# Optimization experiments

Hardware: AMD Instinct MI355X
Metric: run time of the kernel (lower is better)

Reference implementation:

```python
import jax, jax.numpy as jnp
import numpy as np

HEADS = 8
DIM_HEAD = 32
EPS = 1e-5


def setup_inputs() -> dict:
    key = jax.random.key(0)
    ks = jax.random.split(key, 12)
    b, dim, H, W = 16, 256, 64, 64
    led = 128
    hid = HEADS * DIM_HEAD
    return {
        "x": jax.random.normal(ks[0], (b, dim, H, W), dtype=jnp.float32),
        "condition": jax.random.normal(ks[1], (b, led), dtype=jnp.float32),
        "w_qkv": jax.random.normal(ks[2], (3 * hid, dim), dtype=jnp.float32) * 0.02,
        "w_lk": jax.random.normal(ks[3], (hid, led), dtype=jnp.float32) * 0.02,
        "b_lk": jax.random.normal(ks[4], (hid,), dtype=jnp.float32) * 0.02,
        "w_lq": jax.random.normal(ks[5], (hid, led), dtype=jnp.float32) * 0.02,
        "b_lq": jax.random.normal(ks[6], (hid,), dtype=jnp.float32) * 0.02,
        "w_out": jax.random.normal(ks[7], (dim, hid), dtype=jnp.float32) * 0.02,
        "b_out": jax.random.normal(ks[8], (dim,), dtype=jnp.float32) * 0.02,
        "gn_gamma": jnp.ones((dim,), dtype=jnp.float32),
        "gn_beta": jnp.zeros((dim,), dtype=jnp.float32),
    }


def reference(x, condition, w_qkv, w_lk, b_lk, w_lq, b_lq, w_out, b_out, gn_gamma, gn_beta):
    b, c, H, W = x.shape
    n = H * W
    scale = DIM_HEAD ** (-0.5)
    hid = HEADS * DIM_HEAD

    # 1x1 conv QKV projection (no bias)
    qkv = jnp.einsum('oc,bchw->bohw', w_qkv, x)  # [b, 3*hid, H, W]
    qkv = qkv.reshape(b, 3, HEADS, DIM_HEAD, n)
    q, k, v = qkv[:, 0], qkv[:, 1], qkv[:, 2]     # each [b, heads, d, n]

    # conditioning biases
    lk = (condition @ w_lk.T + b_lk).reshape(b, HEADS, DIM_HEAD, 1)
    lq = (condition @ w_lq.T + b_lq).reshape(b, HEADS, DIM_HEAD, 1)
    k = k + lk
    q = q + lq

    # double softmax (linear attention)
    q = jax.nn.softmax(q, axis=-2) * scale  # over feature dim d
    k = jax.nn.softmax(k, axis=-1)          # over spatial dim n

    context = jnp.einsum('bhdn,bhen->bhde', k, v)   # [b, h, d, e]
    out = jnp.einsum('bhde,bhdn->bhen', context, q)  # [b, h, e, n]
    out = out.reshape(b, hid, H, W)

    # to_out: 1x1 conv + bias, then GroupNorm(1, dim)
    y = jnp.einsum('oc,bchw->bohw', w_out, out) + b_out[None, :, None, None]
    mean = jnp.mean(y, axis=(1, 2, 3), keepdims=True)
    var = jnp.var(y, axis=(1, 2, 3), keepdims=True)
    y = (y - mean) * jax.lax.rsqrt(var + EPS)
    return y * gn_gamma[None, :, None, None] + gn_beta[None, :, None, None]
```

## Files before the change

kernel.cpp:

```cpp
#include <hip/hip_runtime.h>


#define NB    16
#define DIM   256
#define NSP   4096
#define LED   128
#define HID   256
#define NHEAD 8
#define SCALE 0.17677669529663687f

typedef __bf16 bf16x8 __attribute__((ext_vector_type(8)));
typedef float f32x4 __attribute__((ext_vector_type(4)));
typedef unsigned short us8 __attribute__((ext_vector_type(8)));
typedef unsigned short us4 __attribute__((ext_vector_type(4)));

__device__ __forceinline__ unsigned short f2bf(float f){
  unsigned u = __builtin_bit_cast(unsigned, f);
  u += 0x7fffu + ((u >> 16) & 1u);
  return (unsigned short)(u >> 16);
}
__device__ __forceinline__ float bf2f(unsigned short h){
  unsigned u = ((unsigned)h) << 16;
  return __builtin_bit_cast(float, u);
}
__device__ __forceinline__ bf16x8 ldb8(const unsigned short* p){
  us8 r = *(const us8*)p;
  return __builtin_bit_cast(bf16x8, r);
}
__device__ __forceinline__ f32x4 mfma16(bf16x8 a, bf16x8 b, f32x4 c){
  return __builtin_amdgcn_mfma_f32_16x16x32_bf16(a, b, c, 0, 0, 0);
}
__device__ __forceinline__ void gl16(const unsigned short* g, unsigned short* l){
  __builtin_amdgcn_global_load_lds(
      (const __attribute__((address_space(1))) unsigned int*)g,
      (__attribute__((address_space(3))) unsigned int*)l,
      16, 0, 0);
}

__global__ __launch_bounds__(256) void k0_prep(
    const float* __restrict__ wqkv, const float* __restrict__ cond,
    const float* __restrict__ wlk, const float* __restrict__ blk,
    const float* __restrict__ wlq, const float* __restrict__ blq,
    unsigned short* __restrict__ whi,
    float* __restrict__ lk, float* __restrict__ lq)
{
  const int idx = blockIdx.x*256 + threadIdx.x;
  if (idx < 768*256){
    whi[idx] = f2bf(wqkv[idx]);
  } else {
    int i = idx - 768*256;
    const int which = (i >= NB*HID) ? 1 : 0;
    i &= (NB*HID - 1);
    const int b = i >> 8, o = i & 255;
    const float* wm = which ? wlq : wlk;
    const float* bs = which ? blq : blk;
    float s = bs[o];
    const float* c = cond + b*LED;
    const float* wr = wm + o*LED;
    for (int j=0;j<LED;j++) s += c[j]*wr[j];
    (which ? lq : lk)[i] = s;
  }
}

__global__ __launch_bounds__(256) void k1_txpose(
    const float* __restrict__ x, unsigned short* __restrict__ xt)
{
  __shared__ float tile[64][65];
  const int c0 = blockIdx.x*64, n0 = blockIdx.y*64, b = blockIdx.z;
  const int t = threadIdx.x;
  const int tr = t >> 6, tc = t & 63;
  const float* xp = x + ((size_t)b*DIM + c0)*NSP + n0;
  #pragma unroll
  for (int i=0;i<16;i++){
    const int cl = i*4 + tr;
    tile[cl][tc] = xp[(size_t)cl*NSP + tc];
  }
  __syncthreads();
  unsigned short* xtp = xt + ((size_t)b*NSP + n0)*DIM + c0;
  #pragma unroll
  for (int pass=0; pass<2; pass++){
    const int nl = pass*32 + (t>>3);
    const int c8 = (t&7)*8;
    us8 v;
    #pragma unroll
    for (int j=0;j<8;j++) v[j] = f2bf(tile[c8+j][nl]);
    *(us8*)&xtp[(size_t)nl*DIM + c8] = v;
  }
}

__global__ __launch_bounds__(256) void k2_gemm1(
    const unsigned short* __restrict__ whi,
    const unsigned short* __restrict__ xt,
    const float* __restrict__ lkv, const float* __restrict__ lqv,
    unsigned short* __restrict__ qh,
    unsigned short* __restrict__ kexp, unsigned short* __restrict__ vout,
    float* __restrict__ ksum)
{
  __shared__ __align__(16) unsigned char smraw[32768];
  unsigned short* Ah  = (unsigned short*)smraw;
  unsigned short* Bt  = (unsigned short*)(smraw + 16384);
  unsigned short* stg = (unsigned short*)smraw;

  const int nt = blockIdx.x, mt = blockIdx.y, b = blockIdx.z;
  const int o0 = mt*128, n0 = nt*128;
  const int t = threadIdx.x, lane = t & 63, wv = t >> 6;
  const int wr = wv >> 1, wc = wv & 1;
  const int cl = lane & 15, g = lane >> 4;

  f32x4 acc[4][4];
  const f32x4 z4 = {0.f,0.f,0.f,0.f};
  #pragma unroll
  for (int m=0;m<4;m++)
    #pragma unroll
    for (int n=0;n<4;n++) acc[m][n] = z4;

  const unsigned short* xb = xt + ((size_t)b*NSP + n0)*DIM;
  const int rowc = lane >> 3;
  const int gcol = 8*((lane & 7) ^ rowc);

  for (int kt=0; kt<4; kt++){
    const int k0 = kt*64;
    __syncthreads();
    #pragma unroll
    for (int j=0;j<4;j++){
      const int rg = wv*4 + j;
      const int rr = rg*8 + rowc;
      gl16(&whi[(size_t)(o0+rr)*DIM + k0 + gcol], &Ah[rg*512]);
      gl16(&xb [(size_t)rr*DIM      + k0 + gcol], &Bt[rg*512]);
    }
    __syncthreads();
    #pragma unroll
    for (int kk=0; kk<2; kk++){
      const int ko = kk*32 + g*8;
      const int kosw = ko ^ ((cl & 7) << 3);
      bf16x8 a1[4], bb[4];
      #pragma unroll
      for (int m=0;m<4;m++)
        a1[m] = ldb8(&Ah[(wr*64 + m*16 + cl)*64 + kosw]);
      #pragma unroll
      for (int n=0;n<4;n++)
        bb[n] = ldb8(&Bt[(wc*64 + n*16 + cl)*64 + kosw]);
      #pragma unroll
      for (int m=0;m<4;m++)
        #pragma unroll
        for (int n=0;n<4;n++)
          acc[m][n] = mfma16(a1[m], bb[n], acc[m][n]);
    }
  }

  __syncthreads();

  if (mt < 2){
    float lqr[4][4];
    #pragma unroll
    for (int m=0;m<4;m++)
      #pragma unroll
      for (int i=0;i<4;i++)
        lqr[m][i] = lqv[b*HID + o0 + wr*64 + m*16 + g*4 + i];
    #pragma unroll
    for (int j=0;j<2;j++){
      #pragma unroll
      for (int nf=0;nf<4;nf++){
        float e[8]; float mx = -1e30f;
        #pragma unroll
        for (int mm=0;mm<2;mm++)
          #pragma unroll
          for (int i=0;i<4;i++){
            const int m = 2*j+mm;
            const float v = acc[m][nf][i] + lqr[m][i];
            e[mm*4+i] = v; mx = fmaxf(mx, v);
          }
        mx = fmaxf(mx, __shfl_xor(mx, 16));
        mx = fmaxf(mx, __shfl_xor(mx, 32));
        float s = 0.f;
        #pragma unroll
        for (int q2=0;q2<8;q2++){ e[q2] = __expf(e[q2]-mx); s += e[q2]; }
        s += __shfl_xor(s, 16);
        s += __shfl_xor(s, 32);
        const float r = 1.f/s;
        const int n_local = wc*64 + nf*16 + cl;
        const int rsw = (n_local & 7) << 3;
        #pragma unroll
        for (int mm=0;mm<2;mm++){
          const int dg_local = wr*64 + (2*j+mm)*16 + g*4;
          us4 h4;
          #pragma unroll
          for (int i=0;i<4;i++) h4[i] = f2bf(e[mm*4+i]*r);
          *(us4*)&stg[n_local*128 + (dg_local ^ rsw)] = h4;
        }
      }
    }
    __syncthreads();
    unsigned short* qbase = qh + ((size_t)b*NSP + n0)*HID + o0;
    #pragma unroll
    for (int i2=0;i2<8;i2++){
      const int n_local = wv*32 + i2*4 + (lane>>4);
      const int dg8 = (lane&15)*8;
      us8 val = *(const us8*)&stg[n_local*128 + (dg8 ^ ((n_local&7)<<3))];
      *(us8*)&qbase[(size_t)n_local*HID + dg8] = val;
    }
  } else {
    const int isK = (mt < 4);
    const int dgbase = isK ? (mt-2)*128 : (mt-4)*128;
    #pragma unroll
    for (int m=0;m<4;m++)
      #pragma unroll
      for (int i=0;i<4;i++){
        const int dg_local = wr*64 + m*16 + g*4 + i;
        const int nb0 = wc*64 + cl;
        const int rsw = (dg_local & 7) << 3;
        if (isK){
          const float lkval = lkv[b*HID + dgbase + dg_local];
          float s = 0.f;
          #pragma unroll
          for (int nf=0;nf<4;nf++){
            const float v = __expf(acc[m][nf][i] + lkval);
            const unsigned short hh = f2bf(v);
            stg[dg_local*128 + ((nb0 + nf*16) ^ rsw)] = hh;
            s += bf2f(hh);
          }
          s += __shfl_xor(s,1); s += __shfl_xor(s,2);
          s += __shfl_xor(s,4); s += __shfl_xor(s,8);
          if (cl == 0) atomicAdd(&ksum[b*HID + dgbase + dg_local], s);
        } else {
          #pragma unroll
          for (int nf=0;nf<4;nf++)
            stg[dg_local*128 + ((nb0 + nf*16) ^ rsw)] = f2bf(acc[m][nf][i]);
        }
      }
    __syncthreads();
    unsigned short* obase = (isK ? kexp : vout) + ((size_t)b*HID + dgbase)*NSP + n0;
    #pragma unroll
    for (int i2=0;i2<8;i2++){
      const int dg_local = wv*32 + i2*4 + (lane>>4);
      const int n8 = (lane&15)*8;
      us8 val = *(const us8*)&stg[dg_local*128 + (n8 ^ ((dg_local&7)<<3))];
      *(us8*)&obase[(size_t)dg_local*NSP + n8] = val;
    }
  }
}

__global__ __launch_bounds__(256) void k3_ctx(
    const unsigned short* __restrict__ kexp, const unsigned short* __restrict__ vv,
    float* __restrict__ ctxp)
{
  const int half = blockIdx.x, h = blockIdx.y, b = blockIdx.z;
  const int t = threadIdx.x, lane = t&63, wv = t>>6;
  const int cl = lane&15, g = lane>>4;
  const int nstart = half*2048 + wv*512;
  f32x4 acc[2][2];
  const f32x4 z4 = {0.f,0.f,0.f,0.f};
  acc[0][0]=z4; acc[0][1]=z4; acc[1][0]=z4; acc[1][1]=z4;
  const unsigned short* kb = kexp + ((size_t)b*HID + h*32)*NSP;
  const unsigned short* vb = vv   + ((size_t)b*HID + h*32)*NSP;
  for (int ks=0; ks<16; ks++){
    const int k = nstart + ks*32 + g*8;
    bf16x8 a0 = ldb8(&kb[(size_t)(cl)   *NSP + k]);
    bf16x8 a1 = ldb8(&kb[(size_t)(16+cl)*NSP + k]);
    bf16x8 b0 = ldb8(&vb[(size_t)(cl)   *NSP + k]);
    bf16x8 b1 = ldb8(&vb[(size_t)(16+cl)*NSP + k]);
    acc[0][0] = mfma16(a0,b0,acc[0][0]);
    acc[0][1] = mfma16(a0,b1,acc[0][1]);
    acc[1][0] = mfma16(a1,b0,acc[1][0]);
    acc[1][1] = mfma16(a1,b1,acc[1][1]);
  }
  float* outp = ctxp + ((((size_t)b*NHEAD + h)*2 + half)*4 + wv)*1024;
  #pragma unroll
  for (int dm=0;dm<2;dm++)
    #pragma unroll
    for (int em=0;em<2;em++)
      #pragma unroll
      for (int i=0;i<4;i++)
        outp[(dm*16 + g*4 + i)*32 + em*16 + cl] = acc[dm][em][i];
}

__global__ __launch_bounds__(256) void k4_m(
    const float* __restrict__ ctxp, const float* __restrict__ ksum,
    const float* __restrict__ wout,
    unsigned short* __restrict__ mhi)
{
  const int h = blockIdx.x, b = blockIdx.y;
  __shared__ float ctxl[32][32];
  __shared__ float rkn[32];
  const int t = threadIdx.x;
  const float* base = ctxp + (((size_t)b*NHEAD + h)*8)*1024;
  #pragma unroll
  for (int r=0;r<4;r++){
    const int de = r*256 + t;
    float s = 0.f;
    #pragma unroll
    for (int p=0;p<8;p++) s += base[p*1024 + de];
    ctxl[de>>5][de&31] = s;
  }
  if (t < 32) rkn[t] = SCALE / ksum[b*HID + h*32 + t];
  __syncthreads();
  float w[32];
  const float* wrow = wout + (size_t)t*HID + h*32;
  #pragma unroll
  for (int el=0;el<32;el++) w[el] = wrow[el];
  for (int dl=0; dl<32; dl++){
    float s = 0.f;
    #pragma unroll
    for (int el=0;el<32;el++) s += w[el]*ctxl[dl][el];
    s *= rkn[dl];
    mhi[((size_t)b*HID + t)*HID + h*32 + dl] = f2bf(s);
  }
}

__global__ __launch_bounds__(256) void k5a_stats(
    const unsigned short* __restrict__ mhi,
    const unsigned short* __restrict__ qhp, const float* __restrict__ bout,
    float* __restrict__ bsum, float* __restrict__ bssq)
{
  __shared__ __align__(16) unsigned char smraw[32768];
  unsigned short* Ah = (unsigned short*)smraw;
  unsigned short* Bh = (unsigned short*)(smraw + 16384);
  __shared__ float red[8];

  const int nt = blockIdx.x, mt = blockIdx.y, b = blockIdx.z;
  const int o0 = mt*128, n0 = nt*128;
  const int t = threadIdx.x, lane = t&63, wv = t>>6;
  const int wr = wv>>1, wc = wv&1;
  const int cl = lane&15, g = lane>>4;

  f32x4 acc[4][4];
  const f32x4 z4 = {0.f,0.f,0.f,0.f};
  #pragma unroll
  for (int m=0;m<4;m++)
    #pragma unroll
    for (int n=0;n<4;n++) acc[m][n] = z4;

  const unsigned short* ab_h = mhi + (size_t)b*HID*HID;
  const unsigned short* bb_h = qhp + ((size_t)b*NSP + n0)*HID;
  const int rowc = lane >> 3;
  const int gcol = 8*((lane & 7) ^ rowc);

  for (int kt=0; kt<4; kt++){
    const int k0 = kt*64;
    __syncthreads();
    #pragma unroll
    for (int j=0;j<4;j++){
      const int rg = wv*4 + j;
      const int rr = rg*8 + rowc;
      gl16(&ab_h[(size_t)(o0+rr)*HID + k0 + gcol], &Ah[rg*512]);
      gl16(&bb_h[(size_t)rr*HID      + k0 + gcol], &Bh[rg*512]);
    }
    __syncthreads();
    #pragma unroll
    for (int kk=0;kk<2;kk++){
      const int ko = kk*32 + g*8;
      const int kosw = ko ^ ((cl & 7) << 3);
      bf16x8 ah[4], bh[4];
      #pragma unroll
      for (int m=0;m<4;m++)
        ah[m] = ldb8(&Ah[(wr*64 + m*16 + cl)*64 + kosw]);
      #pragma unroll
      for (int n=0;n<4;n++)
        bh[n] = ldb8(&Bh[(wc*64 + n*16 + cl)*64 + kosw]);
      #pragma unroll
      for (int m=0;m<4;m++)
        #pragma unroll
        for (int n=0;n<4;n++)
          acc[m][n] = mfma16(ah[m], bh[n], acc[m][n]);
    }
  }

  float lsum = 0.f, lss = 0.f;
  #pragma unroll
  for (int m=0;m<4;m++)
    #pragma unroll
    for (int i=0;i<4;i++){
      const float bo = bout[o0 + wr*64 + m*16 + g*4 + i];
      #pragma unroll
      for (int nf=0;nf<4;nf++){
        const float v = acc[m][nf][i] + bo;
        lsum += v; lss += v*v;
      }
    }
  #pragma unroll
  for (int sft=1; sft<64; sft<<=1){
    lsum += __shfl_xor(lsum, sft);
    lss  += __shfl_xor(lss,  sft);
  }
  if (lane == 0){ red[wv] = lsum; red[4+wv] = lss; }
  __syncthreads();
  if (t == 0){
    atomicAdd(&bsum[b], red[0]+red[1]+red[2]+red[3]);
    atomicAdd(&bssq[b], red[4]+red[5]+red[6]+red[7]);
  }
}

__global__ __launch_bounds__(256) void k5b_write(
    const unsigned short* __restrict__ mhi,
    const unsigned short* __restrict__ qhp, const float* __restrict__ bout,
    const float* __restrict__ bsum, const float* __restrict__ bssq,
    const float* __restrict__ gamma, const float* __restrict__ beta,
    float* __restrict__ out)
{
  __shared__ __align__(16) unsigned char smraw[32768];
  unsigned short* Ah = (unsigned short*)smraw;
  unsigned short* Bh = (unsigned short*)(smraw + 16384);
  float* stg = (float*)smraw;

  const int nt = blockIdx.x, mt = blockIdx.y, b = blockIdx.z;
  const int o0 = mt*128, n0 = nt*128;
  const int t = threadIdx.x, lane = t&63, wv = t>>6;
  const int wr = wv>>1, wc = wv&1;
  const int cl = lane&15, g = lane>>4;

  f32x4 acc[4][4];
  const f32x4 z4 = {0.f,0.f,0.f,0.f};
  #pragma unroll
  for (int m=0;m<4;m++)
    #pragma unroll
    for (int n=0;n<4;n++) acc[m][n] = z4;

  const unsigned short* ab_h = mhi + (size_t)b*HID*HID;
  const unsigned short* bb_h = qhp + ((size_t)b*NSP + n0)*HID;
  const int rowc = lane >> 3;
  const int gcol = 8*((lane & 7) ^ rowc);

  for (int kt=0; kt<4; kt++){
    const int k0 = kt*64;
    __syncthreads();
    #pragma unroll
    for (int j=0;j<4;j++){
      const int rg = wv*4 + j;
      const int rr = rg*8 + rowc;
      gl16(&ab_h[(size_t)(o0+rr)*HID + k0 + gcol], &Ah[rg*512]);
      gl16(&bb_h[(size_t)rr*HID      + k0 + gcol], &Bh[rg*512]);
    }
    __syncthreads();
    #pragma unroll
    for (int kk=0;kk<2;kk++){
      const int ko = kk*32 + g*8;
      const int kosw = ko ^ ((cl & 7) << 3);
      bf16x8 ah[4], bh[4];
      #pragma unroll
      for (int m=0;m<4;m++)
        ah[m] = ldb8(&Ah[(wr*64 + m*16 + cl)*64 + kosw]);
      #pragma unroll
      for (int n=0;n<4;n++)
        bh[n] = ldb8(&Bh[(wc*64 + n*16 + cl)*64 + kosw]);
      #pragma unroll
      for (int m=0;m<4;m++)
        #pragma unroll
        for (int n=0;n<4;n++)
          acc[m][n] = mfma16(ah[m], bh[n], acc[m][n]);
    }
  }

  const float inv = 1.f/1048576.f;
  const float mean = bsum[b]*inv;
  const float var  = bssq[b]*inv - mean*mean;
  const float ri = rsqrtf(var + 1e-5f);
  float gav[4][4], bev[4][4];
  #pragma unroll
  for (int m=0;m<4;m++)
    #pragma unroll
    for (int i=0;i<4;i++){
      const int o = o0 + wr*64 + m*16 + g*4 + i;
      const float ga = gamma[o]*ri;
      gav[m][i] = ga;
      bev[m][i] = beta[o] + (bout[o]-mean)*ga;
    }

  #pragma unroll
  for (int p=0;p<2;p++){
    __syncthreads();
    #pragma unroll
    for (int mm=0;mm<2;mm++){
      const int m = 2*p+mm;
      #pragma unroll
      for (int nf=0;nf<4;nf++)
        #pragma unroll
        for (int i=0;i<4;i++){
          const int lr = wr*32 + mm*16 + g*4 + i;
          const int col = wc*64 + nf*16 + cl;
          stg[lr*128 + (col ^ ((lr&7)<<2))] = acc[m][nf][i]*gav[m][i] + bev[m][i];
        }
    }
    __syncthreads();
    #pragma unroll
    for (int i2=0;i2<8;i2++){
      const int lr = wv*16 + i2*2 + (lane>>5);
      const int colw = (lane&31)*4;
      f32x4 v = *(const f32x4*)&stg[lr*128 + (colw ^ ((lr&7)<<2))];
      const int dg = o0 + (lr>>5)*64 + p*32 + (lr&31);
      *(f32x4*)&out[((size_t)b*HID + dg)*NSP + n0 + colw] = v;
    }
  }
}

#define OFF_XT     0ull
#define OFF_QH     33554432ull
#define OFF_CTXP   67108864ull
#define OFF_MH     71303168ull
#define OFF_LK     73400320ull
#define OFF_LQ     73416704ull
#define OFF_WHI    73433088ull
#define OFF_KSUM   73826304ull
#define OFF_BSUM   73842688ull
#define OFF_BSSQ   73842752ull

extern "C" void kernel_launch(void* const* d_in, const int* in_sizes, int n_in,
                              void* d_out, int out_size, void* d_ws, size_t ws_size,
                              hipStream_t stream) {
  const float* x     = (const float*)d_in[0];
  const float* cond  = (const float*)d_in[1];
  const float* wqkv  = (const float*)d_in[2];
  const float* wlk   = (const float*)d_in[3];
  const float* blk   = (const float*)d_in[4];
  const float* wlq   = (const float*)d_in[5];
  const float* blq   = (const float*)d_in[6];
  const float* wout  = (const float*)d_in[7];
  const float* bout  = (const float*)d_in[8];
  const float* gamma = (const float*)d_in[9];
  const float* beta  = (const float*)d_in[10];

  char* ws = (char*)d_ws;
  unsigned short* xt   = (unsigned short*)(ws + OFF_XT);
  unsigned short* qh   = (unsigned short*)(ws + OFF_QH);
  float*          ctxp = (float*)(ws + OFF_CTXP);
  unsigned short* mhi  = (unsigned short*)(ws + OFF_MH);
  float*          lk   = (float*)(ws + OFF_LK);
  float*          lq   = (float*)(ws + OFF_LQ);
  unsigned short* whi  = (unsigned short*)(ws + OFF_WHI);
  float*          ksum = (float*)(ws + OFF_KSUM);
  float*          bsum = (float*)(ws + OFF_BSUM);
  float*          bssq = (float*)(ws + OFF_BSSQ);

  unsigned short* kexp = (unsigned short*)d_out;
  unsigned short* vscr = (unsigned short*)d_out + 16777216;
  float*          y    = (float*)d_out;

  hipMemsetAsync(ws + OFF_KSUM, 0, 16384 + 128, stream);

  k0_prep  <<<800, 256, 0, stream>>>(wqkv, cond, wlk, blk, wlq, blq, whi, lk, lq);
  k1_txpose<<<dim3(4,64,16), 256, 0, stream>>>(x, xt);
  k2_gemm1 <<<dim3(32,6,16), 256, 0, stream>>>(whi, xt, lk, lq, qh, kexp, vscr, ksum);
  k3_ctx   <<<dim3(2,8,16), 256, 0, stream>>>(kexp, vscr, ctxp);
  k4_m     <<<dim3(8,16), 256, 0, stream>>>(ctxp, ksum, wout, mhi);
  k5a_stats<<<dim3(32,2,16), 256, 0, stream>>>(mhi, qh, bout, bsum, bssq);
  k5b_write<<<dim3(32,2,16), 256, 0, stream>>>(mhi, qh, bout, bsum, bssq, gamma, beta, y);
}
```

Baseline: 154.4 us.

## Double-buffer LDS tiles with K=32 steps in three GEMM kernels

Replaces the single-buffered K=64 staging loop in the QKV GEMM, stats GEMM and write GEMM with a two-buffer K=32 pipeline. The next tile's global-to-LDS load is issued before the MFMAs on the current buffer, and a new XOR swizzle fits the narrower 32-column rows. This aims to overlap global load latency with compute and cut one barrier per step. In exchange it doubles the loop trip count and relies on the async load completing before the barrier.

```diff
diff --git a/kernel.cpp b/kernel.cpp
--- a/kernel.cpp
+++ b/kernel.cpp
@@ -97,8 +97,6 @@
     float* __restrict__ ksum)
 {
   __shared__ __align__(16) unsigned char smraw[32768];
-  unsigned short* Ah  = (unsigned short*)smraw;
-  unsigned short* Bt  = (unsigned short*)(smraw + 16384);
   unsigned short* stg = (unsigned short*)smraw;
 
   const int nt = blockIdx.x, mt = blockIdx.y, b = blockIdx.z;
@@ -115,40 +113,43 @@
     for (int n=0;n<4;n++) acc[m][n] = z4;
 
   const unsigned short* xb = xt + ((size_t)b*NSP + n0)*DIM;
-  const int rowc = lane >> 3;
-  const int gcol = 8*((lane & 7) ^ rowc);
-
-  for (int kt=0; kt<4; kt++){
-    const int k0 = kt*64;
-    __syncthreads();
-    #pragma unroll
-    for (int j=0;j<4;j++){
-      const int rg = wv*4 + j;
-      const int rr = rg*8 + rowc;
-      gl16(&whi[(size_t)(o0+rr)*DIM + k0 + gcol], &Ah[rg*512]);
-      gl16(&xb [(size_t)rr*DIM      + k0 + gcol], &Bt[rg*512]);
-    }
-    __syncthreads();
-    #pragma unroll
-    for (int kk=0; kk<2; kk++){
-      const int ko = kk*32 + g*8;
-      const int kosw = ko ^ ((cl & 7) << 3);
-      bf16x8 a1[4], bb[4];
-      #pragma unroll
-      for (int m=0;m<4;m++)
-        a1[m] = ldb8(&Ah[(wr*64 + m*16 + cl)*64 + kosw]);
+  const int gc = (((lane&3) ^ ((lane>>2)&3) ^ ((lane>>4)&3)) << 3);
+  const int lrow = lane >> 2;
+  const int psw = ((g ^ (cl&3) ^ (cl>>2)) << 3);
+
+  auto stage = [&](int kt, int sel){
+    unsigned short* Ab = (unsigned short*)(smraw + sel*16384);
+    unsigned short* Bb = Ab + 4096;
+    const int k0 = kt*32;
+    #pragma unroll
+    for (int j=0;j<2;j++){
+      const int rg = wv*2 + j;
+      const int rr = rg*16 + lrow;
+      gl16(&whi[(size_t)(o0+rr)*DIM + k0 + gc], &Ab[rg*512]);
+      gl16(&xb [(size_t)rr*DIM      + k0 + gc], &Bb[rg*512]);
+    }
+  };
+
+  stage(0, 0);
+  __syncthreads();
+  for (int kt=0; kt<8; kt++){
+    if (kt < 7) stage(kt+1, (kt+1)&1);
+    const unsigned short* Ab = (const unsigned short*)(smraw + (kt&1)*16384);
+    const unsigned short* Bb = Ab + 4096;
+    bf16x8 a1[4], bb[4];
+    #pragma unroll
+    for (int m=0;m<4;m++)
+      a1[m] = ldb8(&Ab[(wr*64 + m*16 + cl)*32 + psw]);
+    #pragma unroll
+    for (int n=0;n<4;n++)
+      bb[n] = ldb8(&Bb[(wc*64 + n*16 + cl)*32 + psw]);
+    #pragma unroll
+    for (int m=0;m<4;m++)
       #pragma unroll
       for (int n=0;n<4;n++)
-        bb[n] = ldb8(&Bt[(wc*64 + n*16 + cl)*64 + kosw]);
-      #pragma unroll
-      for (int m=0;m<4;m++)
-        #pragma unroll
-        for (int n=0;n<4;n++)
-          acc[m][n] = mfma16(a1[m], bb[n], acc[m][n]);
-    }
-  }
-
-  __syncthreads();
+        acc[m][n] = mfma16(a1[m], bb[n], acc[m][n]);
+    __syncthreads();
+  }
 
   if (mt < 2){
     float lqr[4][4];
@@ -313,8 +314,6 @@
     float* __restrict__ bsum, float* __restrict__ bssq)
 {
   __shared__ __align__(16) unsigned char smraw[32768];
-  unsigned short* Ah = (unsigned short*)smraw;
-  unsigned short* Bh = (unsigned short*)(smraw + 16384);
   __shared__ float red[8];
 
   const int nt = blockIdx.x, mt = blockIdx.y, b = blockIdx.z;
@@ -332,37 +331,42 @@
 
   const unsigned short* ab_h = mhi + (size_t)b*HID*HID;
   const unsigned short* bb_h = qhp + ((size_t)b*NSP + n0)*HID;
-  const int rowc = lane >> 3;
-  const int gcol = 8*((lane & 7) ^ rowc);
-
-  for (int kt=0; kt<4; kt++){
-    const int k0 = kt*64;
-    __syncthreads();
-    #pragma unroll
-    for (int j=0;j<4;j++){
-      const int rg = wv*4 + j;
-      const int rr = rg*8 + rowc;
-      gl16(&ab_h[(size_t)(o0+rr)*HID + k0 + gcol], &Ah[rg*512]);
-      gl16(&bb_h[(size_t)rr*HID      + k0 + gcol], &Bh[rg*512]);
-    }
-    __syncthreads();
-    #pragma unroll
-    for (int kk=0;kk<2;kk++){
-      const int ko = kk*32 + g*8;
-      const int kosw = ko ^ ((cl & 7) << 3);
-      bf16x8 ah[4], bh[4];
-      #pragma unroll
-      for (int m=0;m<4;m++)
-        ah[m] = ldb8(&Ah[(wr*64 + m*16 + cl)*64 + kosw]);
+  const int gc = (((lane&3) ^ ((lane>>2)&3) ^ ((lane>>4)&3)) << 3);
+  const int lrow = lane >> 2;
+  const int psw = ((g ^ (cl&3) ^ (cl>>2)) << 3);
+
+  auto stage = [&](int kt, int sel){
+    unsigned short* Ab = (unsigned short*)(smraw + sel*16384);
+    unsigned short* Bb = Ab + 4096;
+    const int k0 = kt*32;
+    #pragma unroll
+    for (int j=0;j<2;j++){
+      const int rg = wv*2 + j;
+      const int rr = rg*16 + lrow;
+      gl16(&ab_h[(size_t)(o0+rr)*HID + k0 + gc], &Ab[rg*512]);
+      gl16(&bb_h[(size_t)rr*HID      + k0 + gc], &Bb[rg*512]);
+    }
+  };
+
+  stage(0, 0);
+  __syncthreads();
+  for (int kt=0; kt<8; kt++){
+    if (kt < 7) stage(kt+1, (kt+1)&1);
+    const unsigned short* Ab = (const unsigned short*)(smraw + (kt&1)*16384);
+    const unsigned short* Bb = Ab + 4096;
+    bf16x8 ah[4], bh[4];
+    #pragma unroll
+    for (int m=0;m<4;m++)
+      ah[m] = ldb8(&Ab[(wr*64 + m*16 + cl)*32 + psw]);
+    #pragma unroll
+    for (int n=0;n<4;n++)
+      bh[n] = ldb8(&Bb[(wc*64 + n*16 + cl)*32 + psw]);
+    #pragma unroll
+    for (int m=0;m<4;m++)
       #pragma unroll
       for (int n=0;n<4;n++)
-        bh[n] = ldb8(&Bh[(wc*64 + n*16 + cl)*64 + kosw]);
-      #pragma unroll
-      for (int m=0;m<4;m++)
-        #pragma unroll
-        for (int n=0;n<4;n++)
-          acc[m][n] = mfma16(ah[m], bh[n], acc[m][n]);
-    }
+        acc[m][n] = mfma16(ah[m], bh[n], acc[m][n]);
+    __syncthreads();
   }
 
   float lsum = 0.f, lss = 0.f;
@@ -398,8 +402,6 @@
     float* __restrict__ out)
 {
   __shared__ __align__(16) unsigned char smraw[32768];
-  unsigned short* Ah = (unsigned short*)smraw;
-  unsigned short* Bh = (unsigned short*)(smraw + 16384);
   float* stg = (float*)smraw;
 
   const int nt = blockIdx.x, mt = blockIdx.y, b = blockIdx.z;
@@ -417,37 +419,42 @@
 
   const unsigned short* ab_h = mhi + (size_t)b*HID*HID;
   const unsigned short* bb_h = qhp + ((size_t)b*NSP + n0)*HID;
-  const int rowc = lane >> 3;
-  const int gcol = 8*((lane & 7) ^ rowc);
-
-  for (int kt=0; kt<4; kt++){
-    const int k0 = kt*64;
-    __syncthreads();
-    #pragma unroll
-    for (int j=0;j<4;j++){
-      const int rg = wv*4 + j;
-      const int rr = rg*8 + rowc;
-      gl16(&ab_h[(size_t)(o0+rr)*HID + k0 + gcol], &Ah[rg*512]);
-      gl16(&bb_h[(size_t)rr*HID      + k0 + gcol], &Bh[rg*512]);
-    }
-    __syncthreads();
-    #pragma unroll
-    for (int kk=0;kk<2;kk++){
-      const int ko = kk*32 + g*8;
-      const int kosw = ko ^ ((cl & 7) << 3);
-      bf16x8 ah[4], bh[4];
-      #pragma unroll
-      for (int m=0;m<4;m++)
-        ah[m] = ldb8(&Ah[(wr*64 + m*16 + cl)*64 + kosw]);
+  const int gc = (((lane&3) ^ ((lane>>2)&3) ^ ((lane>>4)&3)) << 3);
+  const int lrow = lane >> 2;
+  const int psw = ((g ^ (cl&3) ^ (cl>>2)) << 3);
+
+  auto stage = [&](int kt, int sel){
+    unsigned short* Ab = (unsigned short*)(smraw + sel*16384);
+    unsigned short* Bb = Ab + 4096;
+    const int k0 = kt*32;
+    #pragma unroll
+    for (int j=0;j<2;j++){
+      const int rg = wv*2 + j;
+      const int rr = rg*16 + lrow;
+      gl16(&ab_h[(size_t)(o0+rr)*HID + k0 + gc], &Ab[rg*512]);
+      gl16(&bb_h[(size_t)rr*HID      + k0 + gc], &Bb[rg*512]);
+    }
+  };
+
+  stage(0, 0);
+  __syncthreads();
+  for (int kt=0; kt<8; kt++){
+    if (kt < 7) stage(kt+1, (kt+1)&1);
+    const unsigned short* Ab = (const unsigned short*)(smraw + (kt&1)*16384);
+    const unsigned short* Bb = Ab + 4096;
+    bf16x8 ah[4], bh[4];
+    #pragma unroll
+    for (int m=0;m<4;m++)
+      ah[m] = ldb8(&Ab[(wr*64 + m*16 + cl)*32 + psw]);
+    #pragma unroll
+    for (int n=0;n<4;n++)
+      bh[n] = ldb8(&Bb[(wc*64 + n*16 + cl)*32 + psw]);
+    #pragma unroll
+    for (int m=0;m<4;m++)
       #pragma unroll
       for (int n=0;n<4;n++)
-        bh[n] = ldb8(&Bh[(wc*64 + n*16 + cl)*64 + kosw]);
-      #pragma unroll
-      for (int m=0;m<4;m++)
-        #pragma unroll
-        for (int n=0;n<4;n++)
-          acc[m][n] = mfma16(ah[m], bh[n], acc[m][n]);
-    }
+        acc[m][n] = mfma16(ah[m], bh[n], acc[m][n]);
+    __syncthreads();
   }
 
   const float inv = 1.f/1048576.f;
```

Result: no change. 157.5 us (+2.0%).

## Fuse K/V projection with context computation, keeping K and V in LDS

Applied to the files above, without the earlier changes.

The fused QKV GEMM is split into a Q-only kernel and a K/V kernel. For each 128-column spatial tile, the K/V kernel computes exp(K) and V, stages both in LDS and immediately forms per-tile partial context matrices with MFMA. This drops the global write and read of the bf16 K and V tensors and removes the separate context kernel. In exchange the context partials grow to 32 per head, which k4 now reduces, and the K/V kernel uses 64 KB of LDS, which lowers occupancy.

```diff
diff --git a/kernel.cpp b/kernel.cpp
--- a/kernel.cpp
+++ b/kernel.cpp
@@ -88,13 +88,11 @@
   }
 }
 
-__global__ __launch_bounds__(256) void k2_gemm1(
+__global__ __launch_bounds__(256) void k2q_gemm1(
     const unsigned short* __restrict__ whi,
     const unsigned short* __restrict__ xt,
-    const float* __restrict__ lkv, const float* __restrict__ lqv,
-    unsigned short* __restrict__ qh,
-    unsigned short* __restrict__ kexp, unsigned short* __restrict__ vout,
-    float* __restrict__ ksum)
+    const float* __restrict__ lqv,
+    unsigned short* __restrict__ qh)
 {
   __shared__ __align__(16) unsigned char smraw[32768];
   unsigned short* Ah  = (unsigned short*)smraw;
@@ -150,128 +148,182 @@
 
   __syncthreads();
 
-  if (mt < 2){
-    float lqr[4][4];
+  float lqr[4][4];
+  #pragma unroll
+  for (int m=0;m<4;m++)
+    #pragma unroll
+    for (int i=0;i<4;i++)
+      lqr[m][i] = lqv[b*HID + o0 + wr*64 + m*16 + g*4 + i];
+  #pragma unroll
+  for (int j=0;j<2;j++){
+    #pragma unroll
+    for (int nf=0;nf<4;nf++){
+      float e[8]; float mx = -1e30f;
+      #pragma unroll
+      for (int mm=0;mm<2;mm++)
+        #pragma unroll
+        for (int i=0;i<4;i++){
+          const int m = 2*j+mm;
+          const float v = acc[m][nf][i] + lqr[m][i];
+          e[mm*4+i] = v; mx = fmaxf(mx, v);
+        }
+      mx = fmaxf(mx, __shfl_xor(mx, 16));
+      mx = fmaxf(mx, __shfl_xor(mx, 32));
+      float s = 0.f;
+      #pragma unroll
+      for (int q2=0;q2<8;q2++){ e[q2] = __expf(e[q2]-mx); s += e[q2]; }
+      s += __shfl_xor(s, 16);
+      s += __shfl_xor(s, 32);
+      const float r = 1.f/s;
+      const int n_local = wc*64 + nf*16 + cl;
+      const int rsw = (n_local & 7) << 3;
+      #pragma unroll
+      for (int mm=0;mm<2;mm++){
+        const int dg_local = wr*64 + (2*j+mm)*16 + g*4;
+        us4 h4;
+        #pragma unroll
+        for (int i=0;i<4;i++) h4[i] = f2bf(e[mm*4+i]*r);
+        *(us4*)&stg[n_local*128 + (dg_local ^ rsw)] = h4;
+      }
+    }
+  }
+  __syncthreads();
+  unsigned short* qbase = qh + ((size_t)b*NSP + n0)*HID + o0;
+  #pragma unroll
+  for (int i2=0;i2<8;i2++){
+    const int n_local = wv*32 + i2*4 + (lane>>4);
+    const int dg8 = (lane&15)*8;
+    us8 val = *(const us8*)&stg[n_local*128 + (dg8 ^ ((n_local&7)<<3))];
+    *(us8*)&qbase[(size_t)n_local*HID + dg8] = val;
+  }
+}
+
+__global__ __launch_bounds__(256) void k2_kv(
+    const unsigned short* __restrict__ whi,
+    const unsigned short* __restrict__ xt,
+    const float* __restrict__ lkv,
+    float* __restrict__ ksum, float* __restrict__ ctxp)
+{
+  __shared__ __align__(16) unsigned char smraw[65536];
+  unsigned short* Abuf = (unsigned short*)smraw;
+  unsigned short* Bbuf = (unsigned short*)(smraw + 16384);
+  unsigned short* Kstg = (unsigned short*)(smraw + 32768);
+  unsigned short* Vstg = (unsigned short*)smraw;
+
+  const int nt = blockIdx.x, hq = blockIdx.y, b = blockIdx.z;
+  const int n0 = nt*128;
+  const int t = threadIdx.x, lane = t & 63, wv = t >> 6;
+  const int wr = wv >> 1, wc = wv & 1;
+  const int cl = lane & 15, g = lane >> 4;
+
+  const unsigned short* xb = xt + ((size_t)b*NSP + n0)*DIM;
+  const int rowc = lane >> 3;
+  const int gcol = 8*((lane & 7) ^ rowc);
+
+  for (int panel=0; panel<2; ++panel){
+    const int prow = 256 + panel*256 + hq*128;
+    f32x4 acc[4][4];
+    const f32x4 z4 = {0.f,0.f,0.f,0.f};
     #pragma unroll
     for (int m=0;m<4;m++)
       #pragma unroll
-      for (int i=0;i<4;i++)
-        lqr[m][i] = lqv[b*HID + o0 + wr*64 + m*16 + g*4 + i];
-    #pragma unroll
-    for (int j=0;j<2;j++){
-      #pragma unroll
-      for (int nf=0;nf<4;nf++){
-        float e[8]; float mx = -1e30f;
-        #pragma unroll
-        for (int mm=0;mm<2;mm++)
+      for (int n=0;n<4;n++) acc[m][n] = z4;
+
+    for (int kt=0; kt<4; kt++){
+      const int k0 = kt*64;
+      __syncthreads();
+      #pragma unroll
+      for (int j=0;j<4;j++){
+        const int rg = wv*4 + j;
+        const int rr = rg*8 + rowc;
+        gl16(&whi[(size_t)(prow+rr)*DIM + k0 + gcol], &Abuf[rg*512]);
+        gl16(&xb [(size_t)rr*DIM       + k0 + gcol], &Bbuf[rg*512]);
+      }
+      __syncthreads();
+      #pragma unroll
+      for (int kk=0; kk<2; kk++){
+        const int ko = kk*32 + g*8;
+        const int kosw = ko ^ ((cl & 7) << 3);
+        bf16x8 a1[4], bb[4];
+        #pragma unroll
+        for (int m=0;m<4;m++)
+          a1[m] = ldb8(&Abuf[(wr*64 + m*16 + cl)*64 + kosw]);
+        #pragma unroll
+        for (int n=0;n<4;n++)
+          bb[n] = ldb8(&Bbuf[(wc*64 + n*16 + cl)*64 + kosw]);
+        #pragma unroll
+        for (int m=0;m<4;m++)
           #pragma unroll
-          for (int i=0;i<4;i++){
-            const int m = 2*j+mm;
-            const float v = acc[m][nf][i] + lqr[m][i];
-            e[mm*4+i] = v; mx = fmaxf(mx, v);
-          }
-        mx = fmaxf(mx, __shfl_xor(mx, 16));
-        mx = fmaxf(mx, __shfl_xor(mx, 32));
-        float s = 0.f;
-        #pragma unroll
-        for (int q2=0;q2<8;q2++){ e[q2] = __expf(e[q2]-mx); s += e[q2]; }
-        s += __shfl_xor(s, 16);
-        s += __shfl_xor(s, 32);
-        const float r = 1.f/s;
-        const int n_local = wc*64 + nf*16 + cl;
-        const int rsw = (n_local & 7) << 3;
-        #pragma unroll
-        for (int mm=0;mm<2;mm++){
-          const int dg_local = wr*64 + (2*j+mm)*16 + g*4;
-          us4 h4;
-          #pragma unroll
-          for (int i=0;i<4;i++) h4[i] = f2bf(e[mm*4+i]*r);
-          *(us4*)&stg[n_local*128 + (dg_local ^ rsw)] = h4;
-        }
+          for (int n=0;n<4;n++)
+            acc[m][n] = mfma16(a1[m], bb[n], acc[m][n]);
       }
     }
     __syncthreads();
-    unsigned short* qbase = qh + ((size_t)b*NSP + n0)*HID + o0;
-    #pragma unroll
-    for (int i2=0;i2<8;i2++){
-      const int n_local = wv*32 + i2*4 + (lane>>4);
-      const int dg8 = (lane&15)*8;
-      us8 val = *(const us8*)&stg[n_local*128 + (dg8 ^ ((n_local&7)<<3))];
-      *(us8*)&qbase[(size_t)n_local*HID + dg8] = val;
-    }
-  } else {
-    const int isK = (mt < 4);
-    const int dgbase = isK ? (mt-2)*128 : (mt-4)*128;
-    #pragma unroll
-    for (int m=0;m<4;m++)
-      #pragma unroll
-      for (int i=0;i<4;i++){
-        const int dg_local = wr*64 + m*16 + g*4 + i;
-        const int nb0 = wc*64 + cl;
-        const int rsw = (dg_local & 7) << 3;
-        if (isK){
-          const float lkval = lkv[b*HID + dgbase + dg_local];
+
+    if (panel == 0){
+      #pragma unroll
+      for (int m=0;m<4;m++)
+        #pragma unroll
+        for (int i=0;i<4;i++){
+          const int row = wr*64 + m*16 + g*4 + i;
+          const float lkval = lkv[b*HID + hq*128 + row];
+          const int rsw = (row & 7) << 3;
           float s = 0.f;
           #pragma unroll
           for (int nf=0;nf<4;nf++){
             const float v = __expf(acc[m][nf][i] + lkval);
             const unsigned short hh = f2bf(v);
-            stg[dg_local*128 + ((nb0 + nf*16) ^ rsw)] = hh;
+            Kstg[row*128 + ((wc*64 + nf*16 + cl) ^ rsw)] = hh;
             s += bf2f(hh);
           }
           s += __shfl_xor(s,1); s += __shfl_xor(s,2);
           s += __shfl_xor(s,4); s += __shfl_xor(s,8);
-          if (cl == 0) atomicAdd(&ksum[b*HID + dgbase + dg_local], s);
-        } else {
+          if (cl == 0) atomicAdd(&ksum[b*HID + hq*128 + row], s);
+        }
+    } else {
+      #pragma unroll
+      for (int m=0;m<4;m++)
+        #pragma unroll
+        for (int i=0;i<4;i++){
+          const int row = wr*64 + m*16 + g*4 + i;
+          const int rsw = (row & 7) << 3;
           #pragma unroll
           for (int nf=0;nf<4;nf++)
-            stg[dg_local*128 + ((nb0 + nf*16) ^ rsw)] = f2bf(acc[m][nf][i]);
+            Vstg[row*128 + ((wc*64 + nf*16 + cl) ^ rsw)] = f2bf(acc[m][nf][i]);
         }
+      __syncthreads();
+      f32x4 cacc[2][2];
+      cacc[0][0]=z4; cacc[0][1]=z4; cacc[1][0]=z4; cacc[1][1]=z4;
+      #pragma unroll
+      for (int ks=0; ks<4; ks++){
+        const int nco = ks*32 + g*8;
+        bf16x8 af[2], bf[2];
+        #pragma unroll
+        for (int d16=0; d16<2; d16++){
+          const int arow = wv*32 + d16*16 + cl;
+          af[d16] = ldb8(&Kstg[arow*128 + (nco ^ ((arow&7)<<3))]);
+        }
+        #pragma unroll
+        for (int e16=0; e16<2; e16++){
+          const int brow = wv*32 + e16*16 + cl;
+          bf[e16] = ldb8(&Vstg[brow*128 + (nco ^ ((brow&7)<<3))]);
+        }
+        #pragma unroll
+        for (int d16=0; d16<2; d16++)
+          #pragma unroll
+          for (int e16=0; e16<2; e16++)
+            cacc[d16][e16] = mfma16(af[d16], bf[e16], cacc[d16][e16]);
       }
-    __syncthreads();
-    unsigned short* obase = (isK ? kexp : vout) + ((size_t)b*HID + dgbase)*NSP + n0;
-    #pragma unroll
-    for (int i2=0;i2<8;i2++){
-      const int dg_local = wv*32 + i2*4 + (lane>>4);
-      const int n8 = (lane&15)*8;
-      us8 val = *(const us8*)&stg[dg_local*128 + (n8 ^ ((dg_local&7)<<3))];
-      *(us8*)&obase[(size_t)dg_local*NSP + n8] = val;
-    }
-  }
-}
-
-__global__ __launch_bounds__(256) void k3_ctx(
-    const unsigned short* __restrict__ kexp, const unsigned short* __restrict__ vv,
-    float* __restrict__ ctxp)
-{
-  const int half = blockIdx.x, h = blockIdx.y, b = blockIdx.z;
-  const int t = threadIdx.x, lane = t&63, wv = t>>6;
-  const int cl = lane&15, g = lane>>4;
-  const int nstart = half*2048 + wv*512;
-  f32x4 acc[2][2];
-  const f32x4 z4 = {0.f,0.f,0.f,0.f};
-  acc[0][0]=z4; acc[0][1]=z4; acc[1][0]=z4; acc[1][1]=z4;
-  const unsigned short* kb = kexp + ((size_t)b*HID + h*32)*NSP;
-  const unsigned short* vb = vv   + ((size_t)b*HID + h*32)*NSP;
-  for (int ks=0; ks<16; ks++){
-    const int k = nstart + ks*32 + g*8;
-    bf16x8 a0 = ldb8(&kb[(size_t)(cl)   *NSP + k]);
-    bf16x8 a1 = ldb8(&kb[(size_t)(16+cl)*NSP + k]);
-    bf16x8 b0 = ldb8(&vb[(size_t)(cl)   *NSP + k]);
-    bf16x8 b1 = ldb8(&vb[(size_t)(16+cl)*NSP + k]);
-    acc[0][0] = mfma16(a0,b0,acc[0][0]);
-    acc[0][1] = mfma16(a0,b1,acc[0][1]);
-    acc[1][0] = mfma16(a1,b0,acc[1][0]);
-    acc[1][1] = mfma16(a1,b1,acc[1][1]);
-  }
-  float* outp = ctxp + ((((size_t)b*NHEAD + h)*2 + half)*4 + wv)*1024;
-  #pragma unroll
-  for (int dm=0;dm<2;dm++)
-    #pragma unroll
-    for (int em=0;em<2;em++)
-      #pragma unroll
-      for (int i=0;i<4;i++)
-        outp[(dm*16 + g*4 + i)*32 + em*16 + cl] = acc[dm][em][i];
+      float* outp = ctxp + ((size_t)((b*NHEAD + hq*4 + wv)*32 + nt))*1024;
+      #pragma unroll
+      for (int d16=0; d16<2; d16++)
+        #pragma unroll
+        for (int e16=0; e16<2; e16++)
+          #pragma unroll
+          for (int i=0;i<4;i++)
+            outp[(d16*16 + g*4 + i)*32 + e16*16 + cl] = cacc[d16][e16][i];
+    }
+  }
 }
 
 __global__ __launch_bounds__(256) void k4_m(
@@ -283,15 +335,11 @@
   __shared__ float ctxl[32][32];
   __shared__ float rkn[32];
   const int t = threadIdx.x;
-  const float* base = ctxp + (((size_t)b*NHEAD + h)*8)*1024;
-  #pragma unroll
-  for (int r=0;r<4;r++){
-    const int de = r*256 + t;
-    float s = 0.f;
-    #pragma unroll
-    for (int p=0;p<8;p++) s += base[p*1024 + de];
-    ctxl[de>>5][de&31] = s;
-  }
+  const float* base = ctxp + ((size_t)(b*NHEAD + h)*32)*1024;
+  f32x4 sacc = {0.f,0.f,0.f,0.f};
+  for (int nt=0; nt<32; nt++)
+    sacc += *(const f32x4*)&base[nt*1024 + t*4];
+  *(f32x4*)&((float*)ctxl)[t*4] = sacc;
   if (t < 32) rkn[t] = SCALE / ksum[b*HID + h*32 + t];
   __syncthreads();
   float w[32];
@@ -495,13 +543,13 @@
 #define OFF_XT     0ull
 #define OFF_QH     33554432ull
 #define OFF_CTXP   67108864ull
-#define OFF_MH     71303168ull
-#define OFF_LK     73400320ull
-#define OFF_LQ     73416704ull
-#define OFF_WHI    73433088ull
-#define OFF_KSUM   73826304ull
-#define OFF_BSUM   73842688ull
-#define OFF_BSSQ   73842752ull
+#define OFF_MH     83886080ull
+#define OFF_LK     85983232ull
+#define OFF_LQ     85999616ull
+#define OFF_WHI    86016000ull
+#define OFF_KSUM   86409216ull
+#define OFF_BSUM   86425600ull
+#define OFF_BSSQ   86425664ull
 
 extern "C" void kernel_launch(void* const* d_in, const int* in_sizes, int n_in,
                               void* d_out, int out_size, void* d_ws, size_t ws_size,
@@ -530,16 +578,14 @@
   float*          bsum = (float*)(ws + OFF_BSUM);
   float*          bssq = (float*)(ws + OFF_BSSQ);
 
-  unsigned short* kexp = (unsigned short*)d_out;
-  unsigned short* vscr = (unsigned short*)d_out + 16777216;
-  float*          y    = (float*)d_out;
+  float* y = (float*)d_out;
 
   hipMemsetAsync(ws + OFF_KSUM, 0, 16384 + 128, stream);
 
   k0_prep  <<<800, 256, 0, stream>>>(wqkv, cond, wlk, blk, wlq, blq, whi, lk, lq);
   k1_txpose<<<dim3(4,64,16), 256, 0, stream>>>(x, xt);
-  k2_gemm1 <<<dim3(32,6,16), 256, 0, stream>>>(whi, xt, lk, lq, qh, kexp, vscr, ksum);
-  k3_ctx   <<<dim3(2,8,16), 256, 0, stream>>>(kexp, vscr, ctxp);
+  k2q_gemm1<<<dim3(32,2,16), 256, 0, stream>>>(whi, xt, lq, qh);
+  k2_kv    <<<dim3(32,2,16), 256, 0, stream>>>(whi, xt, lk, ksum, ctxp);
   k4_m     <<<dim3(8,16), 256, 0, stream>>>(ctxp, ksum, wout, mhi);
   k5a_stats<<<dim3(32,2,16), 256, 0, stream>>>(mhi, qh, bout, bsum, bssq);
   k5b_write<<<dim3(32,2,16), 256, 0, stream>>>(mhi, qh, bout, bsum, bssq, gamma, beta, y);
```

New measurement: 176.7 us. 1.14x slower.
